# Optimization experiments

Hardware: AMD Instinct MI355X
Metric: run time of the kernel (lower is better)

Reference implementation:

```python
import jax, jax.numpy as jnp
import numpy as np

DIL = 2  # dilation of the 3x3 neighborhood (hardcoded in the torch module)
# 8 non-center neighbor offsets of a dilated 3x3 kernel
_OFFSETS = [(-DIL, -DIL), (-DIL, 0), (-DIL, DIL),
            (0, -DIL),              (0, DIL),
            (DIL, -DIL), (DIL, 0),  (DIL, DIL)]


def setup_inputs() -> dict:
    key = jax.random.key(0)
    k1, k2 = jax.random.split(key)
    shape = (16, 1, 1024, 1024)
    y_true = jax.random.uniform(k1, shape, dtype=jnp.float32)
    y_pred = jax.random.uniform(k2, shape, dtype=jnp.float32)
    return {"y_true": y_true, "y_pred": y_pred}


def reference(y_true, y_pred):
    # --- BCE with torch's log clamp at -100 (reduction='none') ---
    log_p  = jnp.maximum(jnp.log(y_pred),   -100.0)
    log_1p = jnp.maximum(jnp.log1p(-y_pred), -100.0)
    a = -(y_true * log_p + (1.0 - y_true) * log_1p)

    # --- detached copy (y_pred.clone().detach()) ---
    sloss = jax.lax.stop_gradient(y_pred)

    # --- max |center - neighbor| over 8 dilated neighbors, zero-padded borders ---
    H, W = sloss.shape[2], sloss.shape[3]
    padded = jnp.pad(sloss, ((0, 0), (0, 0), (DIL, DIL), (DIL, DIL)))
    unfolded_weights = jnp.zeros_like(sloss)
    for dy, dx in _OFFSETS:
        nb = padded[:, :, DIL + dy:DIL + dy + H, DIL + dx:DIL + dx + W]
        unfolded_weights = jnp.maximum(unfolded_weights, jnp.abs(sloss - nb))

    # thred[thred < 0.5] = 0; loss1 uses thred BEFORE the >=0.5 -> 1 assignment
    thred = jnp.where(sloss >= 0.5, sloss, 0.0)
    loss = unfolded_weights * thred + a
    return loss.mean()
```

## Files before the change

kernel.cpp:

```cpp
#include <hip/hip_runtime.h>

#define HH 1024
#define WW 1024
#define NB 16
#define KROWS 8
#define NELEM ((long long)NB * HH * WW)

__device__ __forceinline__ void load_row(const float* __restrict__ rowp, int x0,
                                         bool ledge, bool redge,
                                         int offL, int offR, float w[8]) {
    float2 a = *(const float2*)(rowp + offL);
    float4 b = *(const float4*)(rowp + x0);
    float2 c = *(const float2*)(rowp + offR);
    if (ledge) { a.x = 0.f; a.y = 0.f; }
    if (redge) { c.x = 0.f; c.y = 0.f; }
    w[0]=a.x; w[1]=a.y; w[2]=b.x; w[3]=b.y; w[4]=b.z; w[5]=b.w; w[6]=c.x; w[7]=c.y;
}

__device__ __forceinline__ void zero_row(float w[8]) {
#pragma unroll
    for (int i = 0; i < 8; ++i) w[i] = 0.f;
}

__global__ __launch_bounds__(256) void closs_main(const float* __restrict__ yt,
                                                  const float* __restrict__ yp,
                                                  float* __restrict__ out) {
    const int bid = blockIdx.x;
    const int img = bid >> 7;
    const int rem = bid & 127;
    const int par = rem >> 6;
    const int seg = rem & 63;
    const int y0  = seg * (2 * KROWS) + par;

    const int tid = threadIdx.x;
    const int x0  = tid << 2;
    const bool ledge = (tid == 0);
    const bool redge = (tid == 255);
    const int offL = ledge ? x0 : (x0 - 2);
    const int offR = redge ? x0 : (x0 + 4);

    const float* __restrict__ ybase = yp + (long long)img * (HH * WW);
    const float* __restrict__ tbase = yt + (long long)img * (HH * WW);

    float win[3][8];
    if (y0 >= 2) load_row(ybase + (y0 - 2) * WW, x0, ledge, redge, offL, offR, win[0]);
    else         zero_row(win[0]);
    load_row(ybase + y0 * WW, x0, ledge, redge, offL, offR, win[1]);

    float sum = 0.f;
#pragma unroll
    for (int k = 0; k < KROWS; ++k) {
        const int y = y0 + 2 * k;
        float* A = win[k % 3];
        float* B = win[(k + 1) % 3];
        float* C = win[(k + 2) % 3];
        if (y + 2 < HH) load_row(ybase + (y + 2) * WW, x0, ledge, redge, offL, offR, C);
        else            zero_row(C);

        const float4 t4 = *(const float4*)(tbase + y * WW + x0);
        const float tt[4] = {t4.x, t4.y, t4.z, t4.w};

#pragma unroll
        for (int j = 0; j < 4; ++j) {
            const float c = B[j + 2];
            float mx = fmaxf(fmaxf(A[j], A[j + 2]), A[j + 4]);
            mx = fmaxf(fmaxf(mx, B[j]), B[j + 4]);
            mx = fmaxf(fmaxf(mx, C[j]), C[j + 2]);
            mx = fmaxf(mx, C[j + 4]);
            float mn = fminf(fminf(A[j], A[j + 2]), A[j + 4]);
            mn = fminf(fminf(mn, B[j]), B[j + 4]);
            mn = fminf(fminf(mn, C[j]), C[j + 2]);
            mn = fminf(mn, C[j + 4]);
            const float w = fmaxf(mx - c, c - mn);

            const float lp  = fmaxf(__logf(c), -100.f);
            const float l1p = fmaxf(__logf(1.f - c), -100.f);
            const float a   = -(tt[j] * lp + (1.f - tt[j]) * l1p);
            const float th  = (c >= 0.5f) ? c : 0.f;
            sum += w * th + a;
        }
    }

    for (int o = 32; o > 0; o >>= 1) sum += __shfl_down(sum, o);
    __shared__ float wsum[4];
    if ((tid & 63) == 0) wsum[tid >> 6] = sum;
    __syncthreads();
    if (tid == 0) {
        const float total = wsum[0] + wsum[1] + wsum[2] + wsum[3];
        atomicAdd(out, total * (1.0f / (float)NELEM));
    }
}

extern "C" void kernel_launch(void* const* d_in, const int* in_sizes, int n_in,
                              void* d_out, int out_size, void* d_ws, size_t ws_size,
                              hipStream_t stream) {
    const float* y_true = (const float*)d_in[0];
    const float* y_pred = (const float*)d_in[1];
    float* out = (float*)d_out;

    hipMemsetAsync(out, 0, sizeof(float), stream);
    closs_main<<<NB * 2 * (HH / 2 / KROWS), 256, 0, stream>>>(y_true, y_pred, out);
}
```

Measured before the change: 147.9 us.

## Process one row per block with XCD-aware row mapping instead of sliding window

Each block now handles a single output row, loading the three dilated rows directly rather than sliding a 3-row register window over 8 rows of the same parity. Block ids are swizzled so the eight XCDs each get a contiguous range of rows, which should help the neighbor rows hit in the same L2. The BCE term is rewritten algebraically to save a multiply. The cost is that each y_pred row is now loaded three times from the cache hierarchy instead of once, and the grid grows to 16384 blocks with an atomic per block.

```diff
diff --git a/kernel.cpp b/kernel.cpp
--- a/kernel.cpp
+++ b/kernel.cpp
@@ -3,8 +3,8 @@
 #define HH 1024
 #define WW 1024
 #define NB 16
-#define KROWS 8
-#define NELEM ((long long)NB * HH * WW)
+#define NROWS (NB * HH)
+#define NELEM ((long long)NROWS * WW)
 
 __device__ __forceinline__ void load_row(const float* __restrict__ rowp, int x0,
                                          bool ledge, bool redge,
@@ -26,59 +26,47 @@
                                                   const float* __restrict__ yp,
                                                   float* __restrict__ out) {
     const int bid = blockIdx.x;
-    const int img = bid >> 7;
-    const int rem = bid & 127;
-    const int par = rem >> 6;
-    const int seg = rem & 63;
-    const int y0  = seg * (2 * KROWS) + par;
-
+    const int r   = ((bid & 7) << 11) | (bid >> 3);
+    const int y   = r & (HH - 1);
     const int tid = threadIdx.x;
     const int x0  = tid << 2;
+    const long long rowbase = (long long)r * WW;
+
     const bool ledge = (tid == 0);
     const bool redge = (tid == 255);
     const int offL = ledge ? x0 : (x0 - 2);
     const int offR = redge ? x0 : (x0 + 4);
 
-    const float* __restrict__ ybase = yp + (long long)img * (HH * WW);
-    const float* __restrict__ tbase = yt + (long long)img * (HH * WW);
+    const float* pce = yp + rowbase;
 
-    float win[3][8];
-    if (y0 >= 2) load_row(ybase + (y0 - 2) * WW, x0, ledge, redge, offL, offR, win[0]);
-    else         zero_row(win[0]);
-    load_row(ybase + y0 * WW, x0, ledge, redge, offL, offR, win[1]);
+    float A[8], B[8], C[8];
+    load_row(pce, x0, ledge, redge, offL, offR, B);
+    if (y >= 2) load_row(pce - 2 * WW, x0, ledge, redge, offL, offR, A);
+    else        zero_row(A);
+    if (y < HH - 2) load_row(pce + 2 * WW, x0, ledge, redge, offL, offR, C);
+    else            zero_row(C);
+
+    const float4 t4 = *(const float4*)(yt + rowbase + x0);
+    const float tt[4] = {t4.x, t4.y, t4.z, t4.w};
 
     float sum = 0.f;
 #pragma unroll
-    for (int k = 0; k < KROWS; ++k) {
-        const int y = y0 + 2 * k;
-        float* A = win[k % 3];
-        float* B = win[(k + 1) % 3];
-        float* C = win[(k + 2) % 3];
-        if (y + 2 < HH) load_row(ybase + (y + 2) * WW, x0, ledge, redge, offL, offR, C);
-        else            zero_row(C);
+    for (int j = 0; j < 4; ++j) {
+        const float c = B[j + 2];
+        const float mxA = fmaxf(fmaxf(A[j], A[j + 2]), A[j + 4]);
+        const float mxB = fmaxf(B[j], B[j + 4]);
+        const float mxC = fmaxf(fmaxf(C[j], C[j + 2]), C[j + 4]);
+        const float mx  = fmaxf(fmaxf(mxA, mxB), mxC);
+        const float mnA = fminf(fminf(A[j], A[j + 2]), A[j + 4]);
+        const float mnB = fminf(B[j], B[j + 4]);
+        const float mnC = fminf(fminf(C[j], C[j + 2]), C[j + 4]);
+        const float mn  = fminf(fminf(mnA, mnB), mnC);
+        const float w   = fmaxf(mx - c, c - mn);
 
-        const float4 t4 = *(const float4*)(tbase + y * WW + x0);
-        const float tt[4] = {t4.x, t4.y, t4.z, t4.w};
-
-#pragma unroll
-        for (int j = 0; j < 4; ++j) {
-            const float c = B[j + 2];
-            float mx = fmaxf(fmaxf(A[j], A[j + 2]), A[j + 4]);
-            mx = fmaxf(fmaxf(mx, B[j]), B[j + 4]);
-            mx = fmaxf(fmaxf(mx, C[j]), C[j + 2]);
-            mx = fmaxf(mx, C[j + 4]);
-            float mn = fminf(fminf(A[j], A[j + 2]), A[j + 4]);
-            mn = fminf(fminf(mn, B[j]), B[j + 4]);
-            mn = fminf(fminf(mn, C[j]), C[j + 2]);
-            mn = fminf(mn, C[j + 4]);
-            const float w = fmaxf(mx - c, c - mn);
-
-            const float lp  = fmaxf(__logf(c), -100.f);
-            const float l1p = fmaxf(__logf(1.f - c), -100.f);
-            const float a   = -(tt[j] * lp + (1.f - tt[j]) * l1p);
-            const float th  = (c >= 0.5f) ? c : 0.f;
-            sum += w * th + a;
-        }
+        const float lp  = fmaxf(__logf(c), -100.f);
+        const float l1p = fmaxf(__logf(1.f - c), -100.f);
+        const float th  = (c >= 0.5f) ? c : 0.f;
+        sum += w * th - l1p - tt[j] * (lp - l1p);
     }
 
     for (int o = 32; o > 0; o >>= 1) sum += __shfl_down(sum, o);
@@ -99,5 +87,5 @@
     float* out = (float*)d_out;
 
     hipMemsetAsync(out, 0, sizeof(float), stream);
-    closs_main<<<NB * 2 * (HH / 2 / KROWS), 256, 0, stream>>>(y_true, y_pred, out);
+    closs_main<<<NROWS, 256, 0, stream>>>(y_true, y_pred, out);
 }
```

Result: slower. 320.6 us (+116.7%).
